# Kernel tuning notes

Hardware: AMD Instinct MI355X
Metric: run time of the kernel (lower is better)

## Reference

```python
import jax, jax.numpy as jnp
import numpy as np

# ---- static config (from module code / init_kwargs) ----
D_MODEL = 512
D_STATE = 64
D_CONV = 4
EXPAND = 2
HEADDIM = 64
D_INNER = EXPAND * D_MODEL          # 1024
NHEADS = D_INNER // HEADDIM         # 16
D_IN_PROJ = 2 * D_INNER + 2 * D_STATE + NHEADS  # 2192
CONV_DIM = D_INNER + 2 * D_STATE    # 1152
N_LAYERS = 2
VOCAB = 32768
BATCH = 2
SEQ = 512
EPS = 1e-5


def setup_inputs() -> dict:
    key = jax.random.key(0)
    ks = jax.random.split(key, 12)
    g = lambda k, shape, s=0.02: (jax.random.normal(k, shape, jnp.float32) * s)
    return {
        "input_ids": jax.random.randint(ks[0], (BATCH, SEQ), 0, VOCAB),
        "padding_mask": jnp.zeros((BATCH, SEQ), dtype=bool),  # True = pad
        "embeddings": g(ks[1], (VOCAB, D_MODEL)),
        "in_proj_w": g(ks[2], (N_LAYERS, D_IN_PROJ, D_MODEL)),
        "conv_w": g(ks[3], (N_LAYERS, CONV_DIM, D_CONV), 0.1),
        "conv_b": jnp.zeros((N_LAYERS, CONV_DIM), jnp.float32),
        "dt_bias": g(ks[4], (N_LAYERS, NHEADS), 0.5),
        "A_log": jnp.log(jax.random.uniform(ks[5], (N_LAYERS, NHEADS), jnp.float32, 1.0, 16.0)),
        "D_ssm": jnp.ones((N_LAYERS, NHEADS), jnp.float32),
        "norm_w": jnp.ones((N_LAYERS, D_INNER), jnp.float32),
        "out_proj_w": g(ks[6], (N_LAYERS, D_MODEL, D_INNER)),
        "aggr_w": g(ks[7], (D_MODEL, 2 * D_MODEL)),
        "aggr_b": jnp.zeros((D_MODEL,), jnp.float32),
        "norm_f_w": jnp.ones((D_MODEL,), jnp.float32),
        "lm_head_w": g(ks[8], (VOCAB, D_MODEL)),
        "lm_head_b": jnp.zeros((VOCAB,), jnp.float32),
    }


def rmsnorm(x, w):
    return x * jax.lax.rsqrt(jnp.mean(x * x, axis=-1, keepdims=True) + EPS) * w


def flip_sc(X, padding_mask):
    # reverse the valid (non-pad) prefix of each sequence, leave pad positions in place
    b, l, _ = X.shape
    lengths = jnp.sum(~padding_mask, axis=1)                        # (b,)
    pos = jnp.arange(l)[None, :]                                    # (1,l)
    keep = pos < lengths[:, None]
    rev = jnp.where(keep, lengths[:, None] - 1 - pos, pos)          # (b,l)
    return jnp.take_along_axis(X, rev[:, :, None], axis=1)


def causal_conv(x, w, b):
    # x: (b,l,c); depthwise causal conv with kernel size D_CONV
    xt = jnp.transpose(x, (0, 2, 1))                                # (b,c,l)
    y = jax.lax.conv_general_dilated(
        xt, w[:, None, :], window_strides=(1,), padding=[(D_CONV - 1, 0)],
        feature_group_count=w.shape[0], dimension_numbers=("NCH", "OIH", "NCH"))
    return jnp.transpose(y + b[None, :, None], (0, 2, 1))


def ssd_scan(x, dt, A, B, C):
    # x:(b,l,h,p) dt:(b,l,h) A:(h,) B,C:(b,l,n) -> y:(b,l,h,p)
    bsz = x.shape[0]
    dA = jnp.exp(dt * A)                                            # (b,l,h)
    dtx = dt[..., None] * x                                         # (b,l,h,p)
    def step(h, inp):
        dA_t, dtx_t, B_t, C_t = inp
        h = h * dA_t[:, :, None, None] + dtx_t[..., None] * B_t[:, None, None, :]
        y = jnp.einsum("bhpn,bn->bhp", h, C_t)
        return h, y
    h0 = jnp.zeros((bsz, NHEADS, HEADDIM, D_STATE), x.dtype)
    xs = (jnp.swapaxes(dA, 0, 1), jnp.swapaxes(dtx, 0, 1),
          jnp.swapaxes(B, 0, 1), jnp.swapaxes(C, 0, 1))
    _, ys = jax.lax.scan(step, h0, xs)
    return jnp.swapaxes(ys, 0, 1)


def mamba2_block(x, wi, cw, cb, dtb, alog, dss, nw, wo):
    # Mamba2 layer with residual (EncoderLayer: mamba(X) + X)
    b, l, _ = x.shape
    zxbcdt = jnp.einsum("bld,ed->ble", x, wi)                      # (b,l,D_IN_PROJ)
    z = zxbcdt[..., :D_INNER]
    xBC = zxbcdt[..., D_INNER:D_INNER + CONV_DIM]
    dt = jax.nn.softplus(zxbcdt[..., D_INNER + CONV_DIM:] + dtb)   # (b,l,h)
    xBC = jax.nn.silu(causal_conv(xBC, cw, cb))
    xs = xBC[..., :D_INNER].reshape(b, l, NHEADS, HEADDIM)
    B = xBC[..., D_INNER:D_INNER + D_STATE]
    C = xBC[..., D_INNER + D_STATE:]
    A = -jnp.exp(alog)                                             # (h,)
    y = ssd_scan(xs, dt, A, B, C) + xs * dss[None, None, :, None]
    y = y.reshape(b, l, D_INNER)
    y = rmsnorm(y * jax.nn.silu(z), nw)                            # RMSNormGated
    return jnp.einsum("ble,de->bld", y, wo) + x


def reference(input_ids, padding_mask, embeddings, in_proj_w, conv_w, conv_b,
              dt_bias, A_log, D_ssm, norm_w, out_proj_w, aggr_w, aggr_b,
              norm_f_w, lm_head_w, lm_head_b):
    X = embeddings[input_ids]                                      # (b,l,d)
    for i in range(N_LAYERS):
        X_flip = flip_sc(X, padding_mask)
        X_f = mamba2_block(X, in_proj_w[i], conv_w[i], conv_b[i], dt_bias[i],
                           A_log[i], D_ssm[i], norm_w[i], out_proj_w[i])
        X_b = mamba2_block(X_flip, in_proj_w[i], conv_w[i], conv_b[i], dt_bias[i],
                           A_log[i], D_ssm[i], norm_w[i], out_proj_w[i])
        X_b = flip_sc(X_b, padding_mask)
        # gated bidirectional fusion
        zg = jax.nn.sigmoid(jnp.concatenate([X_f, X_b], axis=-1) @ aggr_w.T + aggr_b)
        X = zg * X_f + (1.0 - zg) * X_b
    h = rmsnorm(X, norm_f_w)
    logits = h @ lm_head_w.T + lm_head_b                            # (b,l,V)
    return logits
```

## Files before the change

kernel.cpp:

```cpp
#include <hip/hip_runtime.h>

#define SEQ    512
#define DM     512
#define DI     1024
#define NH     16
#define DS     64
#define CONVD  1152
#define DPROJ  2192

typedef __attribute__((ext_vector_type(8))) short bf16x8;
typedef __attribute__((ext_vector_type(4))) float floatx4;

__device__ __forceinline__ unsigned int f2bf(float f) {
  unsigned int u = __float_as_uint(f);
  u += 0x7FFFu + ((u >> 16) & 1u);
  return u >> 16;
}
__device__ __forceinline__ ushort4 cvt4(float4 v) {
  ushort4 o;
  o.x = (unsigned short)f2bf(v.x); o.y = (unsigned short)f2bf(v.y);
  o.z = (unsigned short)f2bf(v.z); o.w = (unsigned short)f2bf(v.w);
  return o;
}
__device__ __forceinline__ unsigned int cvtpk(float lo, float hi) {
  unsigned int r;
  asm("v_cvt_pk_bf16_f32 %0, %1, %2" : "=v"(r) : "v"(lo), "v"(hi));
  return r;
}
__device__ __forceinline__ float sigmoidf_(float x) { return 1.f / (1.f + __expf(-x)); }
__device__ __forceinline__ float siluf_(float x) { return x * sigmoidf_(x); }

__device__ __forceinline__ void gl16(const void* g, void* l) {
  __builtin_amdgcn_global_load_lds(
      (const __attribute__((address_space(1))) unsigned int*)g,
      (__attribute__((address_space(3))) unsigned int*)l, 16, 0, 0);
}

template<int BM, int BN, int EPI>
__global__ __launch_bounds__(256) void gemm_bf(
    const short* __restrict__ A, const float* __restrict__ B,
    float* __restrict__ C, const int K, const int Nvalid, const int ldc,
    const float* __restrict__ e0, const float* __restrict__ e1,
    unsigned short* __restrict__ o2)
{
  constexpr int FM = BM / 32, FN = BN / 32;
  constexpr int PA = BM / 32, PB = BN / 32;
  __shared__ short As[BM * 64];
  __shared__ short Bs[BN * 64];
  const int tid = threadIdx.x, lane = tid & 63, wave = tid >> 6;
  const int m0 = blockIdx.y * BM, n0 = blockIdx.x * BN;
  const int wm = (wave >> 1) * (BM / 2), wn = (wave & 1) * (BN / 2);
  const int prow = wave * 8 + (lane >> 3);
  const int schk = ((lane & 7) ^ (prow & 7)) << 3;
  const short* agp = A + (size_t)(m0 + prow) * K + schk;
  short* albase = &As[wave * 8 * 64];
  const int r16 = lane & 15, quad = lane >> 4;

  floatx4 acc[FM][FN];
#pragma unroll
  for (int i = 0; i < FM; i++)
#pragma unroll
    for (int j = 0; j < FN; j++) acc[i][j] = (floatx4)0.f;

  for (int k0 = 0; k0 < K; k0 += 64) {
#pragma unroll
    for (int p = 0; p < PA; ++p)
      gl16(agp + (size_t)p * 32 * K + k0, albase + p * 32 * 64);
#pragma unroll
    for (int p = 0; p < PB; ++p) {
      int brow = n0 + p * 32 + prow;
      brow = (brow < Nvalid) ? brow : (Nvalid - 1);
      const float* src = B + (size_t)brow * K + k0 + schk;
      const float4 f0 = *(const float4*)(src);
      const float4 f1 = *(const float4*)(src + 4);
      int4 w;
      w.x = (int)cvtpk(f0.x, f0.y); w.y = (int)cvtpk(f0.z, f0.w);
      w.z = (int)cvtpk(f1.x, f1.y); w.w = (int)cvtpk(f1.z, f1.w);
      *(int4*)&Bs[wave * 512 + p * 2048 + lane * 8] = w;
    }
    __syncthreads();
#pragma unroll
    for (int kk = 0; kk < 2; ++kk) {
      bf16x8 afr[FM], bfr[FN];
#pragma unroll
      for (int i = 0; i < FM; i++) {
        const int row = wm + i * 16 + r16;
        afr[i] = *(const bf16x8*)&As[row * 64 + (((kk * 4 + quad) ^ (row & 7)) << 3)];
      }
#pragma unroll
      for (int j = 0; j < FN; j++) {
        const int row = wn + j * 16 + r16;
        bfr[j] = *(const bf16x8*)&Bs[row * 64 + (((kk * 4 + quad) ^ (row & 7)) << 3)];
      }
#pragma unroll
      for (int i = 0; i < FM; i++)
#pragma unroll
        for (int j = 0; j < FN; j++)
          acc[i][j] = __builtin_amdgcn_mfma_f32_16x16x32_bf16(afr[i], bfr[j], acc[i][j], 0, 0, 0);
    }
    __syncthreads();
  }

  const int er = quad << 2;
#pragma unroll
  for (int i = 0; i < FM; ++i)
#pragma unroll
    for (int j = 0; j < FN; ++j)
#pragma unroll
      for (int r = 0; r < 4; ++r) {
        const int gm = m0 + wm + i * 16 + er + r;
        const int gn = n0 + wn + j * 16 + r16;
        float v = acc[i][j][r];
        if (EPI == 0) {
          if (gn < Nvalid) C[(size_t)gm * ldc + gn] = v;
        } else if (EPI == 1) {
          const int mm = gm & 1023;
          v += e0[(size_t)mm * DM + gn];
          const size_t idx = (size_t)mm * DI + ((gm >> 10) << 9) + gn;
          C[idx] = v;
          o2[idx] = (unsigned short)f2bf(v);
        } else if (EPI == 2) {
          const float zg = sigmoidf_(v + e0[gn]);
          const float xn = zg * e1[(size_t)gm * DI + gn] +
                           (1.f - zg) * e1[(size_t)gm * DI + DM + gn];
          const size_t idx = (size_t)gm * DM + gn;
          C[idx] = xn;
          o2[idx] = (unsigned short)f2bf(xn);
        } else {
          C[(size_t)gm * ldc + gn] = v + e0[gn];
        }
      }
}

__global__ __launch_bounds__(256) void prep_k(
    const int* __restrict__ ids, const float* __restrict__ emb,
    float* __restrict__ Xf, unsigned short* __restrict__ Xb) {
  const int m = blockIdx.x * 2 + (threadIdx.x >> 7), col = threadIdx.x & 127;
  const int row = ids[m];
  float4 v = ((const float4*)(emb + (size_t)row * DM))[col];
  ((float4*)(Xf + (size_t)m * DM))[col] = v;
  ((ushort4*)(Xb + (size_t)m * DM))[col] = cvt4(v);
}

__global__ __launch_bounds__(256) void conv_k(const float* __restrict__ zx,
    const float* __restrict__ cw, const float* __restrict__ cb,
    const float* __restrict__ dtb, const float* __restrict__ alog,
    float* __restrict__ xact, float* __restrict__ dtt, float* __restrict__ dAt) {
  const int t0 = (blockIdx.x & 31) << 4;
  const int half = blockIdx.x >> 5;
  const int b = blockIdx.y;
  const float* src = zx + (size_t)b * SEQ * DPROJ + DI;
  float* d0 = xact + (size_t)b * SEQ * CONVD;
  float* d1 = xact + (size_t)(2 + b) * SEQ * CONVD;

  for (int cc = 0; cc < 3; ++cc) {
    const int ci = cc * 256 + threadIdx.x;
    if (ci >= 576) break;
    const int c = half * 576 + ci;
    const float w0 = cw[c*4+0], w1 = cw[c*4+1], w2 = cw[c*4+2], w3 = cw[c*4+3];
    const float bias = cb[c];
    float a_[22];
#pragma unroll
    for (int j = 0; j < 22; ++j) {
      const int t = t0 - 3 + j;
      a_[j] = (t >= 0 && t < SEQ) ? src[(size_t)t * DPROJ + c] : 0.f;
    }
#pragma unroll
    for (int tt = 0; tt < 16; ++tt) {
      const float f = bias + w0*a_[tt]   + w1*a_[tt+1] + w2*a_[tt+2] + w3*a_[tt+3];
      const float g = bias + w3*a_[tt+3] + w2*a_[tt+4] + w1*a_[tt+5] + w0*a_[tt+6];
      d0[(size_t)(t0+tt) * CONVD + c] = siluf_(f);
      d1[(size_t)(t0+tt) * CONVD + c] = siluf_(g);
    }
  }
  if (half == 0) {
    const int hh = threadIdx.x >> 4, tt2 = threadIdx.x & 15;
    const int t = t0 + tt2;
    const float v = zx[(size_t)(b * SEQ + t) * DPROJ + 2176 + hh] + dtb[hh];
    const float dt = (v > 15.f) ? v : log1pf(__expf(v));
    const float A = -__expf(alog[hh]);
    dtt[(b * NH + hh) * SEQ + t] = dt;
    dAt[(b * NH + hh) * SEQ + t] = __expf(dt * A);
  }
}

__global__ __launch_bounds__(256, 1) void scan_k(const float* __restrict__ xact,
    const float* __restrict__ dtt, const float* __restrict__ dAt,
    float* __restrict__ yn) {
  const int bid = blockIdx.x;
  const int dir = bid >> 7, b = (bid >> 6) & 1, h = (bid >> 2) & 15;
  const int ph = (bid >> 1) & 1, nh = bid & 1;
  const int tid = threadIdx.x, pl = tid & 31, nq = tid >> 5;
  const int p = ph * 32 + pl, nb = nq << 2;
  const float* __restrict__ src = xact + (size_t)(dir * 2 + b) * SEQ * CONVD;
  const float* __restrict__ dtp = dtt + (b * NH + h) * SEQ;
  const float* __restrict__ dap = dAt + (b * NH + h) * SEQ;
  float* __restrict__ yrow = yn + (size_t)nh * (4 * SEQ * DI)
      + (size_t)(dir * 2 + b) * SEQ * DI + h * 64 + ph * 32;
  __shared__ float yp[2][8][16][33];
  float hs[4] = {0.f, 0.f, 0.f, 0.f};
  int pb = 0;

  for (int c0 = 0; c0 < SEQ; c0 += 16, pb ^= 1) {
#pragma unroll
    for (int s = 0; s < 16; ++s) {
      const int tn = dir ? (SEQ - 1 - (c0 + s)) : (c0 + s);
      const float* row = src + (size_t)tn * CONVD;
      const float dts = dtp[tn];
      const float das = dap[tn];
      const float xv = row[h * 64 + p];
      const float4 b4 = *(const float4*)(row + DI + nh * 32 + nb);
      const float4 c4 = *(const float4*)(row + DI + DS + nh * 32 + nb);
      const float dtx = dts * xv;
      float ya;
      hs[0] = hs[0] * das + dtx * b4.x; ya  = hs[0] * c4.x;
      hs[1] = hs[1] * das + dtx * b4.y; ya += hs[1] * c4.y;
      hs[2] = hs[2] * das + dtx * b4.z; ya += hs[2] * c4.z;
      hs[3] = hs[3] * das + dtx * b4.w; ya += hs[3] * c4.w;
      yp[pb][nq][s][pl] = ya;
    }
    __syncthreads();
    {
      const int rt = tid >> 4, rp = (tid & 15) << 1;
      const int tn = dir ? (SEQ - 1 - (c0 + rt)) : (c0 + rt);
      float s0 = 0.f, s1 = 0.f;
#pragma unroll
      for (int j = 0; j < 8; ++j) { s0 += yp[pb][j][rt][rp]; s1 += yp[pb][j][rt][rp + 1]; }
      float2 o; o.x = s0; o.y = s1;
      *(float2*)&yrow[(size_t)tn * DI + rp] = o;
    }
  }
}

__global__ __launch_bounds__(256) void p2_k(const float* __restrict__ yn,
    const float* __restrict__ xact, const float* __restrict__ zx,
    const float* __restrict__ dss, const float* __restrict__ nw,
    unsigned short* __restrict__ A2b) {
  const int m2 = blockIdx.x;
  const int e4 = threadIdx.x << 2;
  const float4 ya = *(const float4*)(yn + (size_t)m2 * DI + e4);
  const float4 yb = *(const float4*)(yn + (size_t)4 * SEQ * DI + (size_t)m2 * DI + e4);
  const float4 x4 = *(const float4*)(xact + (size_t)m2 * CONVD + e4);
  const float4 z4 = *(const float4*)(zx + (size_t)(m2 & 1023) * DPROJ + e4);
  const float d = dss[e4 >> 6];
  float4 g;
  g.x = (ya.x + yb.x + x4.x * d) * siluf_(z4.x);
  g.y = (ya.y + yb.y + x4.y * d) * siluf_(z4.y);
  g.z = (ya.z + yb.z + x4.z * d) * siluf_(z4.z);
  g.w = (ya.w + yb.w + x4.w * d) * siluf_(z4.w);
  float ss = g.x*g.x + g.y*g.y + g.z*g.z + g.w*g.w;
#pragma unroll
  for (int m = 32; m >= 1; m >>= 1) ss += __shfl_xor(ss, m);
  __shared__ float red[4];
  if ((threadIdx.x & 63) == 0) red[threadIdx.x >> 6] = ss;
  __syncthreads();
  const float tot = red[0] + red[1] + red[2] + red[3];
  const float sc = rsqrtf(tot * (1.f / 1024.f) + 1e-5f);
  const float4 w4 = *(const float4*)(nw + e4);
  float4 o;
  o.x = g.x * sc * w4.x; o.y = g.y * sc * w4.y;
  o.z = g.z * sc * w4.z; o.w = g.w * sc * w4.w;
  ((ushort4*)(A2b + (size_t)m2 * DI))[threadIdx.x] = cvt4(o);
}

__global__ __launch_bounds__(128) void fnorm_k(const float* __restrict__ X,
    const float* __restrict__ w, unsigned short* __restrict__ outb) {
  const int m = blockIdx.x;
  const int e4 = threadIdx.x << 2;
  const float4 x4 = *(const float4*)(X + (size_t)m * DM + e4);
  float ss = x4.x*x4.x + x4.y*x4.y + x4.z*x4.z + x4.w*x4.w;
#pragma unroll
  for (int mm = 32; mm >= 1; mm >>= 1) ss += __shfl_xor(ss, mm);
  __shared__ float red[2];
  if ((threadIdx.x & 63) == 0) red[threadIdx.x >> 6] = ss;
  __syncthreads();
  const float tot = red[0] + red[1];
  const float sc = rsqrtf(tot * (1.f / 512.f) + 1e-5f);
  const float4 w4 = *(const float4*)(w + e4);
  float4 o;
  o.x = x4.x * sc * w4.x; o.y = x4.y * sc * w4.y;
  o.z = x4.z * sc * w4.z; o.w = x4.w * sc * w4.w;
  ((ushort4*)(outb + (size_t)m * DM))[threadIdx.x] = cvt4(o);
}

extern "C" void kernel_launch(void* const* d_in, const int* in_sizes, int n_in,
                              void* d_out, int out_size, void* d_ws, size_t ws_size,
                              hipStream_t stream) {
  (void)in_sizes; (void)n_in; (void)out_size; (void)ws_size;
  const int*   ids  = (const int*)d_in[0];
  const float* emb  = (const float*)d_in[2];
  const float* wi   = (const float*)d_in[3];
  const float* cw   = (const float*)d_in[4];
  const float* cb   = (const float*)d_in[5];
  const float* dtb  = (const float*)d_in[6];
  const float* alog = (const float*)d_in[7];
  const float* dss  = (const float*)d_in[8];
  const float* nw   = (const float*)d_in[9];
  const float* wo   = (const float*)d_in[10];
  const float* aw   = (const float*)d_in[11];
  const float* ab   = (const float*)d_in[12];
  const float* nfw  = (const float*)d_in[13];
  const float* lmw  = (const float*)d_in[14];
  const float* lmb  = (const float*)d_in[15];
  float* out = (float*)d_out;

  float* ws    = (float*)d_ws;
  float* Xf    = ws;
  float* zx    = Xf    + (size_t)524288;
  float* xact  = zx    + (size_t)2244608;
  float* dtt   = xact  + (size_t)2359296;
  float* dAt   = dtt   + (size_t)16384;
  float* yn    = dAt   + (size_t)16384;
  float* Xcatf = yn    + (size_t)4194304;
  unsigned short* Xb    = (unsigned short*)(Xcatf + (size_t)1048576);
  unsigned short* A2b   = Xb    + (size_t)524288;
  unsigned short* Xcatb = A2b   + (size_t)2097152;
  unsigned short* hnb   = Xcatb + (size_t)1048576;

  prep_k<<<dim3(512), dim3(256), 0, stream>>>(ids, emb, Xf, Xb);

  for (int layer = 0; layer < 2; ++layer) {
    gemm_bf<128, 128, 0><<<dim3(18, 8), dim3(256), 0, stream>>>(
        (const short*)Xb, wi + (size_t)layer * DPROJ * DM,
        zx, 512, 2192, 2192, nullptr, nullptr, nullptr);
    conv_k<<<dim3(64, 2), dim3(256), 0, stream>>>(
        zx, cw + (size_t)layer * 4608, cb + (size_t)layer * 1152,
        dtb + 16 * layer, alog + 16 * layer, xact, dtt, dAt);
    scan_k<<<dim3(256), dim3(256), 0, stream>>>(xact, dtt, dAt, yn);
    p2_k<<<dim3(2048), dim3(256), 0, stream>>>(yn, xact, zx, dss + 16 * layer,
                                               nw + (size_t)layer * 1024, A2b);
    gemm_bf<64, 128, 1><<<dim3(4, 32), dim3(256), 0, stream>>>(
        (const short*)A2b, wo + (size_t)layer * DM * DI,
        Xcatf, 1024, 512, 512, Xf, nullptr, Xcatb);
    gemm_bf<64, 64, 2><<<dim3(8, 16), dim3(256), 0, stream>>>(
        (const short*)Xcatb, aw,
        Xf, 1024, 512, 512, ab, Xcatf, Xb);
  }
  fnorm_k<<<dim3(1024), dim3(128), 0, stream>>>(Xf, nfw, hnb);
  gemm_bf<128, 128, 3><<<dim3(256, 8), dim3(256), 0, stream>>>(
      (const short*)hnb, lmw, out, 512, 32768, 32768, lmb, nullptr, nullptr);
}
```

Before: 550.1 us.

## Pre-convert layer weights to bf16 once and XCD-swizzle the LM-head GEMM grid

The prep kernel now also converts the in_proj, out_proj and aggregation weights to bf16 (in_proj padded to 2304 rows), so the per-layer GEMMs load B tiles with direct global-to-LDS copies instead of loading fp32 and converting in registers. The LM-head GEMM keeps fp32 B conversion but uses a 1D grid remapped so that blocks on the same XCD share contiguous N columns, aiming for better L2 reuse. The cost is an extra conversion pass over the weights in a larger prep launch, plus more workspace.

```diff
diff --git a/kernel.cpp b/kernel.cpp
--- a/kernel.cpp
+++ b/kernel.cpp
@@ -7,6 +7,7 @@
 #define DS     64
 #define CONVD  1152
 #define DPROJ  2192
+#define NPADIN 2304
 
 typedef __attribute__((ext_vector_type(8))) short bf16x8;
 typedef __attribute__((ext_vector_type(4))) float floatx4;
@@ -36,9 +37,9 @@
       (__attribute__((address_space(3))) unsigned int*)l, 16, 0, 0);
 }
 
-template<int BM, int BN, int EPI>
+template<int BM, int BN, int EPI, int BF32B, int XSWZ>
 __global__ __launch_bounds__(256) void gemm_bf(
-    const short* __restrict__ A, const float* __restrict__ B,
+    const short* __restrict__ A, const void* __restrict__ B,
     float* __restrict__ C, const int K, const int Nvalid, const int ldc,
     const float* __restrict__ e0, const float* __restrict__ e1,
     unsigned short* __restrict__ o2)
@@ -48,12 +49,22 @@
   __shared__ short As[BM * 64];
   __shared__ short Bs[BN * 64];
   const int tid = threadIdx.x, lane = tid & 63, wave = tid >> 6;
-  const int m0 = blockIdx.y * BM, n0 = blockIdx.x * BN;
+  int m0, n0;
+  if (XSWZ) {
+    const int wg = blockIdx.x;
+    const int xcd = wg & 7, local = wg >> 3;
+    m0 = (local & 7) * BM;
+    n0 = ((xcd << 5) | (local >> 3)) * BN;
+  } else {
+    m0 = blockIdx.y * BM; n0 = blockIdx.x * BN;
+  }
   const int wm = (wave >> 1) * (BM / 2), wn = (wave & 1) * (BN / 2);
   const int prow = wave * 8 + (lane >> 3);
   const int schk = ((lane & 7) ^ (prow & 7)) << 3;
   const short* agp = A + (size_t)(m0 + prow) * K + schk;
+  const short* bgp = (const short*)B + (size_t)(n0 + prow) * K + schk;
   short* albase = &As[wave * 8 * 64];
+  short* blbase = &Bs[wave * 8 * 64];
   const int r16 = lane & 15, quad = lane >> 4;
 
   floatx4 acc[FM][FN];
@@ -66,17 +77,23 @@
 #pragma unroll
     for (int p = 0; p < PA; ++p)
       gl16(agp + (size_t)p * 32 * K + k0, albase + p * 32 * 64);
-#pragma unroll
-    for (int p = 0; p < PB; ++p) {
-      int brow = n0 + p * 32 + prow;
-      brow = (brow < Nvalid) ? brow : (Nvalid - 1);
-      const float* src = B + (size_t)brow * K + k0 + schk;
-      const float4 f0 = *(const float4*)(src);
-      const float4 f1 = *(const float4*)(src + 4);
-      int4 w;
-      w.x = (int)cvtpk(f0.x, f0.y); w.y = (int)cvtpk(f0.z, f0.w);
-      w.z = (int)cvtpk(f1.x, f1.y); w.w = (int)cvtpk(f1.z, f1.w);
-      *(int4*)&Bs[wave * 512 + p * 2048 + lane * 8] = w;
+    if (BF32B == 0) {
+#pragma unroll
+      for (int p = 0; p < PB; ++p)
+        gl16(bgp + (size_t)p * 32 * K + k0, blbase + p * 32 * 64);
+    } else {
+#pragma unroll
+      for (int p = 0; p < PB; ++p) {
+        int brow = n0 + p * 32 + prow;
+        brow = (brow < Nvalid) ? brow : (Nvalid - 1);
+        const float* src = (const float*)B + (size_t)brow * K + k0 + schk;
+        const float4 f0 = *(const float4*)(src);
+        const float4 f1 = *(const float4*)(src + 4);
+        int4 w;
+        w.x = (int)cvtpk(f0.x, f0.y); w.y = (int)cvtpk(f0.z, f0.w);
+        w.z = (int)cvtpk(f1.x, f1.y); w.w = (int)cvtpk(f1.z, f1.w);
+        *(int4*)&Bs[wave * 512 + p * 2048 + lane * 8] = w;
+      }
     }
     __syncthreads();
 #pragma unroll
@@ -132,14 +149,37 @@
       }
 }
 
+#define WO4  262144
+#define AW4  131072
 __global__ __launch_bounds__(256) void prep_k(
     const int* __restrict__ ids, const float* __restrict__ emb,
-    float* __restrict__ Xf, unsigned short* __restrict__ Xb) {
-  const int m = blockIdx.x * 2 + (threadIdx.x >> 7), col = threadIdx.x & 127;
-  const int row = ids[m];
-  float4 v = ((const float4*)(emb + (size_t)row * DM))[col];
-  ((float4*)(Xf + (size_t)m * DM))[col] = v;
-  ((ushort4*)(Xb + (size_t)m * DM))[col] = cvt4(v);
+    const float* __restrict__ wi, const float* __restrict__ wo,
+    const float* __restrict__ aw,
+    float* __restrict__ Xf, unsigned short* __restrict__ Xb,
+    unsigned short* __restrict__ wiB, unsigned short* __restrict__ woB,
+    unsigned short* __restrict__ awB) {
+  const int blk = blockIdx.x, tid = threadIdx.x;
+  if (blk < 512) {
+    const int m = blk * 2 + (tid >> 7), col = tid & 127;
+    const int row = ids[m];
+    float4 v = ((const float4*)(emb + (size_t)row * DM))[col];
+    ((float4*)(Xf + (size_t)m * DM))[col] = v;
+    ((ushort4*)(Xb + (size_t)m * DM))[col] = cvt4(v);
+  } else if (blk < 512 + 2304) {
+    const int slot = (blk - 512) * 2 + (tid >> 7), col = tid & 127;
+    const int l = slot >= 2304 ? 1 : 0;
+    const int row = slot - l * 2304;
+    ushort4 o; o.x = o.y = o.z = o.w = 0;
+    if (row < DPROJ)
+      o = cvt4(((const float4*)(wi + ((size_t)l * DPROJ + row) * DM))[col]);
+    ((ushort4*)(wiB + ((size_t)l * NPADIN + row) * DM))[col] = o;
+  } else {
+    const int i = (blk - 2816) * 256 + tid;
+    if (i < WO4)
+      ((ushort4*)woB)[i] = cvt4(((const float4*)wo)[i]);
+    else
+      ((ushort4*)awB)[i - WO4] = cvt4(((const float4*)aw)[i - WO4]);
+  }
 }
 
 __global__ __launch_bounds__(256) void conv_k(const float* __restrict__ zx,
@@ -316,12 +356,16 @@
   unsigned short* A2b   = Xb    + (size_t)524288;
   unsigned short* Xcatb = A2b   + (size_t)2097152;
   unsigned short* hnb   = Xcatb + (size_t)1048576;
-
-  prep_k<<<dim3(512), dim3(256), 0, stream>>>(ids, emb, Xf, Xb);
+  unsigned short* wiB   = hnb   + (size_t)524288;
+  unsigned short* woB   = wiB   + (size_t)2359296;
+  unsigned short* awB   = woB   + (size_t)1048576;
+
+  prep_k<<<dim3(4352), dim3(256), 0, stream>>>(ids, emb, wi, wo, aw,
+                                               Xf, Xb, wiB, woB, awB);
 
   for (int layer = 0; layer < 2; ++layer) {
-    gemm_bf<128, 128, 0><<<dim3(18, 8), dim3(256), 0, stream>>>(
-        (const short*)Xb, wi + (size_t)layer * DPROJ * DM,
+    gemm_bf<128, 128, 0, 0, 0><<<dim3(18, 8), dim3(256), 0, stream>>>(
+        (const short*)Xb, wiB + (size_t)layer * NPADIN * DM,
         zx, 512, 2192, 2192, nullptr, nullptr, nullptr);
     conv_k<<<dim3(64, 2), dim3(256), 0, stream>>>(
         zx, cw + (size_t)layer * 4608, cb + (size_t)layer * 1152,
@@ -329,14 +373,14 @@
     scan_k<<<dim3(256), dim3(256), 0, stream>>>(xact, dtt, dAt, yn);
     p2_k<<<dim3(2048), dim3(256), 0, stream>>>(yn, xact, zx, dss + 16 * layer,
                                                nw + (size_t)layer * 1024, A2b);
-    gemm_bf<64, 128, 1><<<dim3(4, 32), dim3(256), 0, stream>>>(
-        (const short*)A2b, wo + (size_t)layer * DM * DI,
+    gemm_bf<64, 128, 1, 0, 0><<<dim3(4, 32), dim3(256), 0, stream>>>(
+        (const short*)A2b, woB + (size_t)layer * DM * DI,
         Xcatf, 1024, 512, 512, Xf, nullptr, Xcatb);
-    gemm_bf<64, 64, 2><<<dim3(8, 16), dim3(256), 0, stream>>>(
-        (const short*)Xcatb, aw,
+    gemm_bf<64, 64, 2, 0, 0><<<dim3(8, 16), dim3(256), 0, stream>>>(
+        (const short*)Xcatb, awB,
         Xf, 1024, 512, 512, ab, Xcatf, Xb);
   }
   fnorm_k<<<dim3(1024), dim3(128), 0, stream>>>(Xf, nfw, hnb);
-  gemm_bf<128, 128, 3><<<dim3(256, 8), dim3(256), 0, stream>>>(
+  gemm_bf<128, 128, 3, 1, 1><<<dim3(2048), dim3(256), 0, stream>>>(
       (const short*)hnb, lmw, out, 512, 32768, 32768, lmb, nullptr, nullptr);
 }
```

New measurement: 529.6 us. -3.7%, faster.
